# Performance work log

Hardware: AMD Instinct MI355X
Metric: run time of the kernel (lower is better)

## Reference

```python
import jax, jax.numpy as jnp
import numpy as np

K = 1024        # knowledge_num == feature dim == number of knowledge nodes
E_N = 30000     # exercise_num
E_DIR = 65536
E_UND = 65536
E_EK = 120000


def _uniform(k, shape, scale):
    return jax.random.uniform(k, shape, jnp.float32, -scale, scale)


def setup_inputs() -> dict:
    key = jax.random.key(0)
    ks = jax.random.split(key, 20)
    s = 1.0 / np.sqrt(K)        # nn.Linear default init bound
    s2 = 1.0 / np.sqrt(2 * K)
    return {
        'exer_emb': jax.random.normal(ks[0], (E_N, K), jnp.float32),
        'kn_emb': jax.random.normal(ks[1], (K, K), jnp.float32),
        'dir_src': jax.random.randint(ks[2], (E_DIR,), 0, K),
        'dir_dst': jax.random.randint(ks[3], (E_DIR,), 0, K),
        'und_src': jax.random.randint(ks[4], (E_UND,), 0, K),
        'und_dst': jax.random.randint(ks[5], (E_UND,), 0, K),
        # e_from_k: src are knowledge nodes offset into combined [exer; kn] graph
        'ek_src': jax.random.randint(ks[6], (E_EK,), 0, K) + E_N,
        'ek_dst': jax.random.randint(ks[7], (E_EK,), 0, E_N),
        'W_dir': _uniform(ks[8], (K, K), s),
        'a_dir': _uniform(ks[9], (2 * K,), s2),
        'W_und': _uniform(ks[10], (K, K), s),
        'a_und': _uniform(ks[11], (2 * K,), s2),
        'W_ek': _uniform(ks[12], (K, K), s),
        'a_ek': _uniform(ks[13], (2 * K,), s2),
        'k_w1': _uniform(ks[14], (2 * K,), s2), 'k_b1': _uniform(ks[15], (), s2),
        'k_w2': _uniform(ks[16], (2 * K,), s2), 'k_b2': _uniform(ks[17], (), s2),
        'e_w1': _uniform(ks[18], (2 * K,), s2), 'e_b1': _uniform(ks[19], (), s2),
    }


def gat_layer(h, W, a, src, dst, num_nodes):
    """GraphLayer: z = h@W; e_ij = a^T [z_src, z_dst]; softmax over in-edges; h_i = sum alpha*z_src."""
    z = h @ W                                   # [N, D]
    d = z.shape[1]
    e = (z @ a[:d])[src] + (z @ a[d:])[dst]     # [E] edge logits (split avoids [E,2D] concat)
    m = jax.ops.segment_max(e, dst, num_segments=num_nodes)
    ex = jnp.exp(e - m[dst])
    den = jax.ops.segment_sum(ex, dst, num_segments=num_nodes)
    alpha = ex / den[dst]                       # per-dst softmax (mailbox softmax)
    return jax.ops.segment_sum(alpha[:, None] * z[src], dst, num_segments=num_nodes)


def reference(exer_emb, kn_emb, dir_src, dir_dst, und_src, und_dst, ek_src, ek_dst,
              W_dir, a_dir, W_und, a_und, W_ek, a_ek,
              k_w1, k_b1, k_w2, k_b2, e_w1, e_b1):
    k_directed = gat_layer(kn_emb, W_dir, a_dir, dir_src, dir_dst, K)
    k_undirected = gat_layer(kn_emb, W_und, a_und, und_src, und_dst, K)
    e_k = jnp.concatenate([exer_emb, kn_emb], axis=0)           # [E_N+K, K]
    e_from_k = gat_layer(e_k, W_ek, a_ek, ek_src, ek_dst, E_N + K)

    # knowledge gating: softmax over two concat-linear scores
    A, B, C = kn_emb, k_directed, k_undirected
    s1 = A @ k_w1[:K] + B @ k_w1[K:] + k_b1                     # [K]
    s2 = A @ k_w2[:K] + C @ k_w2[K:] + k_b2
    sc = jax.nn.softmax(jnp.stack([s1, s2], axis=1), axis=1)    # [K, 2]
    kn_out = A + sc[:, 0:1] * B + sc[:, 1:2] * C

    # exercise gating: raw linear score (no softmax)
    Be = e_from_k[:E_N]
    se = exer_emb @ e_w1[:K] + Be @ e_w1[K:] + e_b1             # [E_N]
    exer_out = exer_emb + se[:, None] * Be
    return (exer_out, kn_out)
```

## Files before the change

### kernel.cpp

```cpp
#include <hip/hip_runtime.h>

#define E_N 30000
#define KDIM 1024
#define E_DIRN 65536
#define E_UNDN 65536
#define E_EKN 120000
#define NB (1024 + 1024 + E_N)
#define TOT_E (E_DIRN + E_UNDN + E_EKN)
#define ZERON (3 * KDIM + NB)
#define CAPK 192
#define CAPE 48
#define EKBASE (2048 * CAPK)
#define NEDGE_SLOTS (EKBASE + E_N * CAPE)

typedef __attribute__((ext_vector_type(8))) short bfrag8;
typedef __attribute__((ext_vector_type(4))) float facc4;
typedef __attribute__((ext_vector_type(4))) float f4v;

static __device__ __forceinline__ unsigned short f2bf(float f) {
    unsigned int u = __float_as_uint(f);
    u += 0x7fffu + ((u >> 16) & 1u);
    return (unsigned short)(u >> 16);
}
static __device__ __forceinline__ unsigned int pack2(float lo, float hi) {
    return (unsigned int)f2bf(lo) | ((unsigned int)f2bf(hi) << 16);
}
static __device__ __forceinline__ float bf2f(short u) {
    return __uint_as_float(((unsigned int)(unsigned short)u) << 16);
}
static __device__ __forceinline__ float dot4(f4v a, f4v b) {
    return a.x * b.x + a.y * b.y + a.z * b.z + a.w * b.w;
}
static __device__ __forceinline__ void gload16(const void* g, void* l) {
    __builtin_amdgcn_global_load_lds(
        (const __attribute__((address_space(1))) unsigned int*)g,
        (__attribute__((address_space(3))) unsigned int*)l, 16, 0, 0);
}

__global__ __launch_bounds__(256) void prep(
    const float* __restrict__ kn, const float* __restrict__ W0,
    const float* __restrict__ W1, const float* __restrict__ W2,
    unsigned short* __restrict__ knb, unsigned short* __restrict__ Wtall,
    int* __restrict__ zero_base)
{
    int z = blockIdx.z;
    int tx = threadIdx.x, ty = threadIdx.y;
    if (z == 4) {
        int idx = (blockIdx.y * 32 + blockIdx.x) * 256 + ty * 32 + tx;
        if (idx < ZERON) zero_base[idx] = 0;
        return;
    }
    if (z == 3) {
        int b = blockIdx.y * 32 + blockIdx.x;
        int t = ty * 32 + tx;
        int idx = b * 1024 + t * 4;
        float4 a = *(const float4*)&kn[idx];
        uint2 o; o.x = pack2(a.x, a.y); o.y = pack2(a.z, a.w);
        *(uint2*)&knb[idx] = o;
        return;
    }
    const float* W = (z == 0) ? W0 : (z == 1) ? W1 : W2;
    unsigned short* Wt = Wtall + (size_t)z * KDIM * KDIM;
    __shared__ float tile[32][33];
    int nb = blockIdx.x * 32, kb = blockIdx.y * 32;
#pragma unroll
    for (int r0 = 0; r0 < 32; r0 += 8)
        tile[r0 + ty][tx] = W[(size_t)(kb + r0 + ty) * KDIM + nb + tx];
    __syncthreads();
#pragma unroll
    for (int r0 = 0; r0 < 32; r0 += 8)
        Wt[(size_t)(nb + r0 + ty) * KDIM + kb + tx] = f2bf(tile[tx][r0 + ty]);
}

__global__ __launch_bounds__(256) void gemm_mfma(
    const unsigned short* __restrict__ Ab,
    const unsigned short* __restrict__ Btall,
    const float* __restrict__ a_dir, const float* __restrict__ a_und,
    const float* __restrict__ a_ek,
    unsigned short* __restrict__ Zb, float* __restrict__ zdot)
{
    int z = blockIdx.z;
    const unsigned short* Bb = Btall + (size_t)z * KDIM * KDIM;
    unsigned short* C = Zb + (size_t)z * KDIM * KDIM;
    const float* avec = (z == 0) ? a_dir : (z == 1) ? a_und : a_ek;
    __shared__ alignas(16) unsigned short As[2][64 * 64];
    __shared__ alignas(16) unsigned short Bs[2][128 * 64];
    int tid = threadIdx.x;
    int lane = tid & 63, wv = tid >> 6;
    int wr = wv >> 1, wc = wv & 1;
    int tm = blockIdx.x * 64, tn = blockIdx.y * 128;
    int srow = lane >> 3, sch = lane & 7;
    facc4 acc[2][4] = {};

    auto stage = [&](int buf, int kk) {
#pragma unroll
        for (int t = 0; t < 2; ++t) {
            int r0 = wv * 16 + t * 8;
            int row = r0 + srow;
            gload16(&Ab[(size_t)(tm + row) * KDIM + kk + ((sch ^ (row & 7)) << 3)],
                    &As[buf][r0 * 64]);
        }
#pragma unroll
        for (int t = 0; t < 4; ++t) {
            int r0 = wv * 32 + t * 8;
            int row = r0 + srow;
            gload16(&Bb[(size_t)(tn + row) * KDIM + kk + ((sch ^ (row & 7)) << 3)],
                    &Bs[buf][r0 * 64]);
        }
    };
    auto compute = [&](int buf) {
#pragma unroll
        for (int ks = 0; ks < 2; ++ks) {
            bfrag8 af[2], bfr[4];
            int kch = ks * 4 + (lane >> 4);
#pragma unroll
            for (int f = 0; f < 2; ++f) {
                int ar = wr * 32 + f * 16 + (lane & 15);
                af[f] = *(const bfrag8*)&As[buf][ar * 64 + ((kch ^ (ar & 7)) << 3)];
            }
#pragma unroll
            for (int f = 0; f < 4; ++f) {
                int bcol = wc * 64 + f * 16 + (lane & 15);
                bfr[f] = *(const bfrag8*)&Bs[buf][bcol * 64 + ((kch ^ (bcol & 7)) << 3)];
            }
#pragma unroll
            for (int i = 0; i < 2; ++i)
#pragma unroll
                for (int j = 0; j < 4; ++j)
                    acc[i][j] = __builtin_amdgcn_mfma_f32_16x16x32_bf16(af[i], bfr[j], acc[i][j], 0, 0, 0);
        }
    };

    stage(0, 0);
    __syncthreads();
    int cur = 0;
    for (int kk = 64; kk < KDIM; kk += 64) {
        stage(cur ^ 1, kk);
        compute(cur);
        __syncthreads();
        cur ^= 1;
    }
    compute(cur);

    int col0 = lane & 15, r0 = (lane >> 4) * 4;
    float av4[4];
#pragma unroll
    for (int j = 0; j < 4; ++j) av4[j] = avec[tn + wc * 64 + j * 16 + col0];
#pragma unroll
    for (int i = 0; i < 2; ++i)
#pragma unroll
        for (int j = 0; j < 4; ++j) {
            int row = tm + wr * 32 + i * 16 + r0;
            int col = tn + wc * 64 + j * 16 + col0;
#pragma unroll
            for (int r = 0; r < 4; ++r)
                C[(size_t)(row + r) * KDIM + col] = f2bf(acc[i][j][r]);
        }
#pragma unroll
    for (int i = 0; i < 2; ++i)
#pragma unroll
        for (int r = 0; r < 4; ++r) {
            float t = acc[i][0][r] * av4[0] + acc[i][1][r] * av4[1]
                    + acc[i][2][r] * av4[2] + acc[i][3][r] * av4[3];
            t += __shfl_xor(t, 1); t += __shfl_xor(t, 2);
            t += __shfl_xor(t, 4); t += __shfl_xor(t, 8);
            if ((lane & 15) == 0)
                atomicAdd(&zdot[z * KDIM + tm + wr * 32 + i * 16 + r0 + r], t);
        }
}

__global__ __launch_bounds__(256) void scatter_edges(
    const int* __restrict__ dir_src, const int* __restrict__ dir_dst,
    const int* __restrict__ und_src, const int* __restrict__ und_dst,
    const int* __restrict__ ek_src, const int* __restrict__ ek_dst,
    const float* __restrict__ zdot, int* __restrict__ counts,
    int2* __restrict__ edge_sw)
{
    int i = blockIdx.x * 256 + threadIdx.x;
    int bin, s; float w;
    if (i < E_DIRN) { bin = dir_dst[i]; s = dir_src[i]; w = expf(zdot[s]); }
    else if (i < E_DIRN + E_UNDN) {
        int loc = i - E_DIRN; bin = 1024 + und_dst[loc]; s = und_src[loc]; w = expf(zdot[1024 + s]);
    } else if (i < TOT_E) {
        int loc = i - E_DIRN - E_UNDN; bin = 2048 + ek_dst[loc]; s = ek_src[loc] - E_N; w = expf(zdot[2048 + s]);
    } else return;
    int slot = atomicAdd(&counts[bin], 1);
    if (bin < 2048) {
        if (slot < CAPK) edge_sw[(size_t)bin * CAPK + slot] = make_int2(s, __float_as_int(w));
    } else {
        if (slot < CAPE) edge_sw[EKBASE + (size_t)(bin - 2048) * CAPE + slot] = make_int2(s, __float_as_int(w));
    }
}

__global__ __launch_bounds__(256) void gather_all(
    const unsigned short* __restrict__ Zb, const int2* __restrict__ edge_sw,
    const int* __restrict__ counts,
    const float* __restrict__ exer, const float* __restrict__ kn,
    const float* __restrict__ k_w1, const float* __restrict__ k_b1,
    const float* __restrict__ k_w2, const float* __restrict__ k_b2,
    const float* __restrict__ e_w1, const float* __restrict__ e_b1,
    float* __restrict__ out)
{
    __shared__ float bcs[2][KDIM];
    __shared__ float parts[4];
    int tid = threadIdx.x;
    if (blockIdx.x < KDIM) {
        int row = blockIdx.x;
        int wv = tid >> 6, lane = tid & 63;
        int g = wv >> 1, half = wv & 1;
        int bin = (g << 10) + row;
        int n = min(counts[bin], CAPK);
        size_t start = (size_t)bin * CAPK;
        const bfrag8* Zp = (const bfrag8*)(Zb + (size_t)g * KDIM * KDIM) + half * 64 + lane;
        float b8[8] = {};
        float den = 0.f;
        for (int c0 = 0; c0 < n; c0 += 64) {
            int m = min(64, n - c0);
            int s = 0; float w = 0.f;
            if (lane < m) {
                int2 ew = edge_sw[start + c0 + lane];
                s = ew.x; w = __int_as_float(ew.y);
            }
            int j = 0;
            for (; j + 4 <= m; j += 4) {
                int   s0 = __shfl(s, j), s1 = __shfl(s, j+1), s2 = __shfl(s, j+2), s3 = __shfl(s, j+3);
                float w0 = __shfl(w, j), w1 = __shfl(w, j+1), w2 = __shfl(w, j+2), w3 = __shfl(w, j+3);
                bfrag8 v0 = Zp[(size_t)s0 * 128], v1 = Zp[(size_t)s1 * 128];
                bfrag8 v2 = Zp[(size_t)s2 * 128], v3 = Zp[(size_t)s3 * 128];
#pragma unroll
                for (int k = 0; k < 8; ++k)
                    b8[k] += w0*bf2f(v0[k]) + w1*bf2f(v1[k]) + w2*bf2f(v2[k]) + w3*bf2f(v3[k]);
                den += w0 + w1 + w2 + w3;
            }
            for (; j + 2 <= m; j += 2) {
                int   s0 = __shfl(s, j), s1 = __shfl(s, j+1);
                float w0 = __shfl(w, j), w1 = __shfl(w, j+1);
                bfrag8 v0 = Zp[(size_t)s0 * 128], v1 = Zp[(size_t)s1 * 128];
#pragma unroll
                for (int k = 0; k < 8; ++k) b8[k] += w0*bf2f(v0[k]) + w1*bf2f(v1[k]);
                den += w0 + w1;
            }
            if (j < m) {
                int   s0 = __shfl(s, j);
                float w0 = __shfl(w, j);
                bfrag8 v0 = Zp[(size_t)s0 * 128];
#pragma unroll
                for (int k = 0; k < 8; ++k) b8[k] += w0*bf2f(v0[k]);
                den += w0;
            }
        }
        float inv = (n > 0) ? 1.f / den : 0.f;
#pragma unroll
        for (int k = 0; k < 8; ++k) b8[k] *= inv;
        const float* wvp = g ? k_w2 : k_w1;
        int cb = half * 512 + lane * 8;
        f4v A0 = *(const f4v*)&kn[(size_t)row * KDIM + cb];
        f4v A1 = *(const f4v*)&kn[(size_t)row * KDIM + cb + 4];
        f4v wa0 = *(const f4v*)&wvp[cb];
        f4v wa1 = *(const f4v*)&wvp[cb + 4];
        f4v wb0 = *(const f4v*)&wvp[KDIM + cb];
        f4v wb1 = *(const f4v*)&wvp[KDIM + cb + 4];
        f4v bb0 = {b8[0], b8[1], b8[2], b8[3]};
        f4v bb1 = {b8[4], b8[5], b8[6], b8[7]};
        float p = dot4(A0, wa0) + dot4(A1, wa1) + dot4(bb0, wb0) + dot4(bb1, wb1);
#pragma unroll
        for (int off = 32; off > 0; off >>= 1) p += __shfl_xor(p, off);
        if (lane == 0) parts[wv] = p;
        *(f4v*)&bcs[g][cb] = bb0;
        *(f4v*)&bcs[g][cb + 4] = bb1;
        __syncthreads();
        float s1 = parts[0] + parts[1] + k_b1[0];
        float s2 = parts[2] + parts[3] + k_b2[0];
        float mx = fmaxf(s1, s2);
        float e1 = expf(s1 - mx), e2 = expf(s2 - mx);
        float isum = 1.f / (e1 + e2);
        float sc0 = e1 * isum, sc1 = e2 * isum;
        int col = tid * 4;
        f4v A = *(const f4v*)&kn[(size_t)row * KDIM + col];
        f4v B = *(const f4v*)&bcs[0][col];
        f4v Cc = *(const f4v*)&bcs[1][col];
        *(f4v*)&out[(size_t)(E_N + row) * KDIM + col] = A + sc0 * B + sc1 * Cc;
        return;
    }
    int row = ((blockIdx.x - KDIM) * 256 + tid) >> 6;
    int lane = tid & 63;
    int n = min(counts[2048 + row], CAPE);
    size_t start = EKBASE + (size_t)row * CAPE;
    const f4v* xr = (const f4v*)&exer[(size_t)row * KDIM];
    f4v x00 = __builtin_nontemporal_load(xr + 2 * lane);
    f4v x01 = __builtin_nontemporal_load(xr + 2 * lane + 1);
    f4v x10 = __builtin_nontemporal_load(xr + 2 * lane + 128);
    f4v x11 = __builtin_nontemporal_load(xr + 2 * lane + 129);
    const bfrag8* Zp = (const bfrag8*)(Zb + (size_t)2 * KDIM * KDIM);
    float b0[8] = {}, b1[8] = {};
    float den = 0.f;
    {
        int s = 0; float w = 0.f;
        if (lane < n) {
            int2 ew = edge_sw[start + lane];
            s = ew.x; w = __int_as_float(ew.y);
        }
        int j = 0;
        for (; j + 4 <= n; j += 4) {
            int   s0 = __shfl(s, j), s1 = __shfl(s, j+1), s2 = __shfl(s, j+2), s3 = __shfl(s, j+3);
            float w0 = __shfl(w, j), w1 = __shfl(w, j+1), w2 = __shfl(w, j+2), w3 = __shfl(w, j+3);
            const bfrag8* z0 = Zp + (size_t)s0 * 128;
            const bfrag8* z1 = Zp + (size_t)s1 * 128;
            const bfrag8* z2 = Zp + (size_t)s2 * 128;
            const bfrag8* z3 = Zp + (size_t)s3 * 128;
            bfrag8 a0 = z0[lane], a1 = z0[lane + 64];
            bfrag8 c0v = z1[lane], c1 = z1[lane + 64];
            bfrag8 d0 = z2[lane], d1 = z2[lane + 64];
            bfrag8 e0 = z3[lane], e1 = z3[lane + 64];
#pragma unroll
            for (int k = 0; k < 8; ++k) {
                b0[k] += w0*bf2f(a0[k]) + w1*bf2f(c0v[k]) + w2*bf2f(d0[k]) + w3*bf2f(e0[k]);
                b1[k] += w0*bf2f(a1[k]) + w1*bf2f(c1[k]) + w2*bf2f(d1[k]) + w3*bf2f(e1[k]);
            }
            den += w0 + w1 + w2 + w3;
        }
        for (; j + 2 <= n; j += 2) {
            int   s0 = __shfl(s, j), s1 = __shfl(s, j+1);
            float w0 = __shfl(w, j), w1 = __shfl(w, j+1);
            const bfrag8* z0 = Zp + (size_t)s0 * 128;
            const bfrag8* z1 = Zp + (size_t)s1 * 128;
            bfrag8 a0 = z0[lane], a1 = z0[lane + 64];
            bfrag8 c0v = z1[lane], c1 = z1[lane + 64];
#pragma unroll
            for (int k = 0; k < 8; ++k) {
                b0[k] += w0*bf2f(a0[k]) + w1*bf2f(c0v[k]);
                b1[k] += w0*bf2f(a1[k]) + w1*bf2f(c1[k]);
            }
            den += w0 + w1;
        }
        if (j < n) {
            int   s0 = __shfl(s, j);
            float w0 = __shfl(w, j);
            const bfrag8* z0 = Zp + (size_t)s0 * 128;
            bfrag8 a0 = z0[lane], a1 = z0[lane + 64];
#pragma unroll
            for (int k = 0; k < 8; ++k) {
                b0[k] += w0*bf2f(a0[k]);
                b1[k] += w0*bf2f(a1[k]);
            }
            den += w0;
        }
    }
    float inv = (n > 0) ? 1.f / den : 0.f;
#pragma unroll
    for (int k = 0; k < 8; ++k) { b0[k] *= inv; b1[k] *= inv; }
    const f4v* wap = (const f4v*)e_w1;
    const f4v* wbp = (const f4v*)(e_w1 + KDIM);
    f4v wa0 = wap[2*lane], wa1 = wap[2*lane+1], wa2 = wap[2*lane+128], wa3 = wap[2*lane+129];
    f4v wb0 = wbp[2*lane], wb1 = wbp[2*lane+1], wb2 = wbp[2*lane+128], wb3 = wbp[2*lane+129];
    f4v bb0 = {b0[0], b0[1], b0[2], b0[3]};
    f4v bb1 = {b0[4], b0[5], b0[6], b0[7]};
    f4v bb2 = {b1[0], b1[1], b1[2], b1[3]};
    f4v bb3 = {b1[4], b1[5], b1[6], b1[7]};
    float p = dot4(x00, wa0) + dot4(x01, wa1) + dot4(x10, wa2) + dot4(x11, wa3)
            + dot4(bb0, wb0) + dot4(bb1, wb1) + dot4(bb2, wb2) + dot4(bb3, wb3);
#pragma unroll
    for (int off = 32; off > 0; off >>= 1) p += __shfl_xor(p, off);
    float se = p + e_b1[0];
    f4v* op = (f4v*)&out[(size_t)row * KDIM];
    __builtin_nontemporal_store(x00 + se * bb0, op + 2 * lane);
    __builtin_nontemporal_store(x01 + se * bb1, op + 2 * lane + 1);
    __builtin_nontemporal_store(x10 + se * bb2, op + 2 * lane + 128);
    __builtin_nontemporal_store(x11 + se * bb3, op + 2 * lane + 129);
}

extern "C" void kernel_launch(void* const* d_in, const int* in_sizes, int n_in,
                              void* d_out, int out_size, void* d_ws, size_t ws_size,
                              hipStream_t stream)
{
    (void)in_sizes; (void)n_in; (void)out_size; (void)ws_size;
    const float* exer  = (const float*)d_in[0];
    const float* kn    = (const float*)d_in[1];
    const int* dir_src = (const int*)d_in[2];
    const int* dir_dst = (const int*)d_in[3];
    const int* und_src = (const int*)d_in[4];
    const int* und_dst = (const int*)d_in[5];
    const int* ek_src  = (const int*)d_in[6];
    const int* ek_dst  = (const int*)d_in[7];
    const float* W_dir = (const float*)d_in[8];
    const float* a_dir = (const float*)d_in[9];
    const float* W_und = (const float*)d_in[10];
    const float* a_und = (const float*)d_in[11];
    const float* W_ek  = (const float*)d_in[12];
    const float* a_ek  = (const float*)d_in[13];
    const float* k_w1  = (const float*)d_in[14];
    const float* k_b1  = (const float*)d_in[15];
    const float* k_w2  = (const float*)d_in[16];
    const float* k_b2  = (const float*)d_in[17];
    const float* e_w1  = (const float*)d_in[18];
    const float* e_b1  = (const float*)d_in[19];

    char* ws = (char*)d_ws;
    unsigned short* Zb = (unsigned short*)ws; ws += (size_t)3 * KDIM * KDIM * 2;
    float* zdot    = (float*)ws; ws += 3 * KDIM * 4;
    int* counts    = (int*)ws;   ws += NB * 4;
    int2* edge_sw  = (int2*)ws;  ws += (size_t)NEDGE_SLOTS * 8;
    unsigned short* knb = (unsigned short*)ws; ws += (size_t)KDIM * KDIM * 2;
    unsigned short* Wtb = (unsigned short*)ws; ws += (size_t)3 * KDIM * KDIM * 2;

    prep<<<dim3(32, 32, 5), dim3(32, 8), 0, stream>>>(kn, W_dir, W_und, W_ek,
                                                      knb, Wtb, (int*)zdot);
    gemm_mfma<<<dim3(16, 8, 3), 256, 0, stream>>>(knb, Wtb, a_dir, a_und, a_ek,
                                                  Zb, zdot);
    int eb = (TOT_E + 255) / 256;
    scatter_edges<<<eb, 256, 0, stream>>>(dir_src, dir_dst, und_src, und_dst,
                                          ek_src, ek_dst, zdot, counts, edge_sw);

    float* out = (float*)d_out;
    gather_all<<<KDIM + 7500, 256, 0, stream>>>(Zb, edge_sw, counts,
                                                exer, kn, k_w1, k_b1, k_w2, k_b2,
                                                e_w1, e_b1, out);
}
```

Baseline: 133.0 us.

## Process two exercise rows per wave and read edge pairs as int4 with prefetch

The gather kernel now loads edge (src, weight) pairs two at a time as int4 straight from memory, prefetching the next pair, in place of the lane-load plus shuffle broadcast scheme. This applies to both the knowledge and the exercise paths. Each wave in the exercise path now handles two rows at once, which halves the grid and gives more independent loads in flight per wave. The cost is higher register pressure and divergence when the two rows have different edge counts, plus a dependent serial chain of edge loads.

```diff
diff --git a/kernel.cpp b/kernel.cpp
--- a/kernel.cpp
+++ b/kernel.cpp
@@ -210,42 +210,26 @@
         int g = wv >> 1, half = wv & 1;
         int bin = (g << 10) + row;
         int n = min(counts[bin], CAPK);
-        size_t start = (size_t)bin * CAPK;
+        const int4* ep = (const int4*)(edge_sw + (size_t)bin * CAPK);
         const bfrag8* Zp = (const bfrag8*)(Zb + (size_t)g * KDIM * KDIM) + half * 64 + lane;
         float b8[8] = {};
         float den = 0.f;
-        for (int c0 = 0; c0 < n; c0 += 64) {
-            int m = min(64, n - c0);
-            int s = 0; float w = 0.f;
-            if (lane < m) {
-                int2 ew = edge_sw[start + c0 + lane];
-                s = ew.x; w = __int_as_float(ew.y);
-            }
-            int j = 0;
-            for (; j + 4 <= m; j += 4) {
-                int   s0 = __shfl(s, j), s1 = __shfl(s, j+1), s2 = __shfl(s, j+2), s3 = __shfl(s, j+3);
-                float w0 = __shfl(w, j), w1 = __shfl(w, j+1), w2 = __shfl(w, j+2), w3 = __shfl(w, j+3);
-                bfrag8 v0 = Zp[(size_t)s0 * 128], v1 = Zp[(size_t)s1 * 128];
-                bfrag8 v2 = Zp[(size_t)s2 * 128], v3 = Zp[(size_t)s3 * 128];
-#pragma unroll
-                for (int k = 0; k < 8; ++k)
-                    b8[k] += w0*bf2f(v0[k]) + w1*bf2f(v1[k]) + w2*bf2f(v2[k]) + w3*bf2f(v3[k]);
-                den += w0 + w1 + w2 + w3;
-            }
-            for (; j + 2 <= m; j += 2) {
-                int   s0 = __shfl(s, j), s1 = __shfl(s, j+1);
-                float w0 = __shfl(w, j), w1 = __shfl(w, j+1);
-                bfrag8 v0 = Zp[(size_t)s0 * 128], v1 = Zp[(size_t)s1 * 128];
-#pragma unroll
-                for (int k = 0; k < 8; ++k) b8[k] += w0*bf2f(v0[k]) + w1*bf2f(v1[k]);
+        int np = (n + 1) >> 1;
+        int4 cur = (np > 0) ? ep[0] : make_int4(0, 0, 0, 0);
+        for (int j = 0; j < np; ++j) {
+            int4 c = cur;
+            if (j + 1 < np) cur = ep[j + 1];
+            int s0 = c.x; float w0 = __int_as_float(c.y);
+            bfrag8 v0 = Zp[(size_t)s0 * 128];
+            if (2 * j + 1 < n) {
+                int s1 = c.z; float w1 = __int_as_float(c.w);
+                bfrag8 v1 = Zp[(size_t)s1 * 128];
+#pragma unroll
+                for (int k = 0; k < 8; ++k) b8[k] += w0 * bf2f(v0[k]) + w1 * bf2f(v1[k]);
                 den += w0 + w1;
-            }
-            if (j < m) {
-                int   s0 = __shfl(s, j);
-                float w0 = __shfl(w, j);
-                bfrag8 v0 = Zp[(size_t)s0 * 128];
-#pragma unroll
-                for (int k = 0; k < 8; ++k) b8[k] += w0*bf2f(v0[k]);
+            } else {
+#pragma unroll
+                for (int k = 0; k < 8; ++k) b8[k] += w0 * bf2f(v0[k]);
                 den += w0;
             }
         }
@@ -282,91 +266,118 @@
         *(f4v*)&out[(size_t)(E_N + row) * KDIM + col] = A + sc0 * B + sc1 * Cc;
         return;
     }
-    int row = ((blockIdx.x - KDIM) * 256 + tid) >> 6;
+    int pair = ((blockIdx.x - KDIM) * 256 + tid) >> 6;
     int lane = tid & 63;
-    int n = min(counts[2048 + row], CAPE);
-    size_t start = EKBASE + (size_t)row * CAPE;
-    const f4v* xr = (const f4v*)&exer[(size_t)row * KDIM];
-    f4v x00 = __builtin_nontemporal_load(xr + 2 * lane);
-    f4v x01 = __builtin_nontemporal_load(xr + 2 * lane + 1);
-    f4v x10 = __builtin_nontemporal_load(xr + 2 * lane + 128);
-    f4v x11 = __builtin_nontemporal_load(xr + 2 * lane + 129);
+    int rA = pair * 2, rB = rA + 1;
+    int nA = min(counts[2048 + rA], CAPE);
+    int nB = min(counts[2048 + rB], CAPE);
+    const int4* eA = (const int4*)(edge_sw + EKBASE + (size_t)rA * CAPE);
+    const int4* eB = (const int4*)(edge_sw + EKBASE + (size_t)rB * CAPE);
+    int npA = (nA + 1) >> 1, npB = (nB + 1) >> 1;
+    int npm = max(npA, npB);
+    int4 curA = (npA > 0) ? eA[0] : make_int4(0, 0, 0, 0);
+    int4 curB = (npB > 0) ? eB[0] : make_int4(0, 0, 0, 0);
+    const f4v* xrA = (const f4v*)&exer[(size_t)rA * KDIM];
+    const f4v* xrB = (const f4v*)&exer[(size_t)rB * KDIM];
+    f4v xA0 = __builtin_nontemporal_load(xrA + 2 * lane);
+    f4v xA1 = __builtin_nontemporal_load(xrA + 2 * lane + 1);
+    f4v xA2 = __builtin_nontemporal_load(xrA + 2 * lane + 128);
+    f4v xA3 = __builtin_nontemporal_load(xrA + 2 * lane + 129);
+    f4v xB0 = __builtin_nontemporal_load(xrB + 2 * lane);
+    f4v xB1 = __builtin_nontemporal_load(xrB + 2 * lane + 1);
+    f4v xB2 = __builtin_nontemporal_load(xrB + 2 * lane + 128);
+    f4v xB3 = __builtin_nontemporal_load(xrB + 2 * lane + 129);
     const bfrag8* Zp = (const bfrag8*)(Zb + (size_t)2 * KDIM * KDIM);
-    float b0[8] = {}, b1[8] = {};
-    float den = 0.f;
-    {
-        int s = 0; float w = 0.f;
-        if (lane < n) {
-            int2 ew = edge_sw[start + lane];
-            s = ew.x; w = __int_as_float(ew.y);
-        }
-        int j = 0;
-        for (; j + 4 <= n; j += 4) {
-            int   s0 = __shfl(s, j), s1 = __shfl(s, j+1), s2 = __shfl(s, j+2), s3 = __shfl(s, j+3);
-            float w0 = __shfl(w, j), w1 = __shfl(w, j+1), w2 = __shfl(w, j+2), w3 = __shfl(w, j+3);
+    float a0[8] = {}, a1[8] = {}, b0[8] = {}, b1[8] = {};
+    float denA = 0.f, denB = 0.f;
+    for (int j = 0; j < npm; ++j) {
+        int4 cA = curA, cB = curB;
+        if (j + 1 < npA) curA = eA[j + 1];
+        if (j + 1 < npB) curB = eB[j + 1];
+        if (j < npA) {
+            int s0 = cA.x; float w0 = __int_as_float(cA.y);
             const bfrag8* z0 = Zp + (size_t)s0 * 128;
-            const bfrag8* z1 = Zp + (size_t)s1 * 128;
-            const bfrag8* z2 = Zp + (size_t)s2 * 128;
-            const bfrag8* z3 = Zp + (size_t)s3 * 128;
-            bfrag8 a0 = z0[lane], a1 = z0[lane + 64];
-            bfrag8 c0v = z1[lane], c1 = z1[lane + 64];
-            bfrag8 d0 = z2[lane], d1 = z2[lane + 64];
-            bfrag8 e0 = z3[lane], e1 = z3[lane + 64];
-#pragma unroll
-            for (int k = 0; k < 8; ++k) {
-                b0[k] += w0*bf2f(a0[k]) + w1*bf2f(c0v[k]) + w2*bf2f(d0[k]) + w3*bf2f(e0[k]);
-                b1[k] += w0*bf2f(a1[k]) + w1*bf2f(c1[k]) + w2*bf2f(d1[k]) + w3*bf2f(e1[k]);
+            bfrag8 v00 = z0[lane], v01 = z0[lane + 64];
+            if (2 * j + 1 < nA) {
+                int s1 = cA.z; float w1 = __int_as_float(cA.w);
+                const bfrag8* z1 = Zp + (size_t)s1 * 128;
+                bfrag8 v10 = z1[lane], v11 = z1[lane + 64];
+#pragma unroll
+                for (int k = 0; k < 8; ++k) {
+                    a0[k] += w0 * bf2f(v00[k]) + w1 * bf2f(v10[k]);
+                    a1[k] += w0 * bf2f(v01[k]) + w1 * bf2f(v11[k]);
+                }
+                denA += w0 + w1;
+            } else {
+#pragma unroll
+                for (int k = 0; k < 8; ++k) {
+                    a0[k] += w0 * bf2f(v00[k]);
+                    a1[k] += w0 * bf2f(v01[k]);
+                }
+                denA += w0;
             }
-            den += w0 + w1 + w2 + w3;
-        }
-        for (; j + 2 <= n; j += 2) {
-            int   s0 = __shfl(s, j), s1 = __shfl(s, j+1);
-            float w0 = __shfl(w, j), w1 = __shfl(w, j+1);
+        }
+        if (j < npB) {
+            int s0 = cB.x; float w0 = __int_as_float(cB.y);
             const bfrag8* z0 = Zp + (size_t)s0 * 128;
-            const bfrag8* z1 = Zp + (size_t)s1 * 128;
-            bfrag8 a0 = z0[lane], a1 = z0[lane + 64];
-            bfrag8 c0v = z1[lane], c1 = z1[lane + 64];
-#pragma unroll
-            for (int k = 0; k < 8; ++k) {
-                b0[k] += w0*bf2f(a0[k]) + w1*bf2f(c0v[k]);
-                b1[k] += w0*bf2f(a1[k]) + w1*bf2f(c1[k]);
+            bfrag8 v00 = z0[lane], v01 = z0[lane + 64];
+            if (2 * j + 1 < nB) {
+                int s1 = cB.z; float w1 = __int_as_float(cB.w);
+                const bfrag8* z1 = Zp + (size_t)s1 * 128;
+                bfrag8 v10 = z1[lane], v11 = z1[lane + 64];
+#pragma unroll
+                for (int k = 0; k < 8; ++k) {
+                    b0[k] += w0 * bf2f(v00[k]) + w1 * bf2f(v10[k]);
+                    b1[k] += w0 * bf2f(v01[k]) + w1 * bf2f(v11[k]);
+                }
+                denB += w0 + w1;
+            } else {
+#pragma unroll
+                for (int k = 0; k < 8; ++k) {
+                    b0[k] += w0 * bf2f(v00[k]);
+                    b1[k] += w0 * bf2f(v01[k]);
+                }
+                denB += w0;
             }
-            den += w0 + w1;
-        }
-        if (j < n) {
-            int   s0 = __shfl(s, j);
-            float w0 = __shfl(w, j);
-            const bfrag8* z0 = Zp + (size_t)s0 * 128;
-            bfrag8 a0 = z0[lane], a1 = z0[lane + 64];
-#pragma unroll
-            for (int k = 0; k < 8; ++k) {
-                b0[k] += w0*bf2f(a0[k]);
-                b1[k] += w0*bf2f(a1[k]);
-            }
-            den += w0;
-        }
-    }
-    float inv = (n > 0) ? 1.f / den : 0.f;
-#pragma unroll
-    for (int k = 0; k < 8; ++k) { b0[k] *= inv; b1[k] *= inv; }
+        }
+    }
+    float invA = (nA > 0) ? 1.f / denA : 0.f;
+    float invB = (nB > 0) ? 1.f / denB : 0.f;
+#pragma unroll
+    for (int k = 0; k < 8; ++k) { a0[k] *= invA; a1[k] *= invA; b0[k] *= invB; b1[k] *= invB; }
     const f4v* wap = (const f4v*)e_w1;
     const f4v* wbp = (const f4v*)(e_w1 + KDIM);
     f4v wa0 = wap[2*lane], wa1 = wap[2*lane+1], wa2 = wap[2*lane+128], wa3 = wap[2*lane+129];
     f4v wb0 = wbp[2*lane], wb1 = wbp[2*lane+1], wb2 = wbp[2*lane+128], wb3 = wbp[2*lane+129];
-    f4v bb0 = {b0[0], b0[1], b0[2], b0[3]};
-    f4v bb1 = {b0[4], b0[5], b0[6], b0[7]};
-    f4v bb2 = {b1[0], b1[1], b1[2], b1[3]};
-    f4v bb3 = {b1[4], b1[5], b1[6], b1[7]};
-    float p = dot4(x00, wa0) + dot4(x01, wa1) + dot4(x10, wa2) + dot4(x11, wa3)
-            + dot4(bb0, wb0) + dot4(bb1, wb1) + dot4(bb2, wb2) + dot4(bb3, wb3);
-#pragma unroll
-    for (int off = 32; off > 0; off >>= 1) p += __shfl_xor(p, off);
-    float se = p + e_b1[0];
-    f4v* op = (f4v*)&out[(size_t)row * KDIM];
-    __builtin_nontemporal_store(x00 + se * bb0, op + 2 * lane);
-    __builtin_nontemporal_store(x01 + se * bb1, op + 2 * lane + 1);
-    __builtin_nontemporal_store(x10 + se * bb2, op + 2 * lane + 128);
-    __builtin_nontemporal_store(x11 + se * bb3, op + 2 * lane + 129);
+    f4v aa0 = {a0[0], a0[1], a0[2], a0[3]};
+    f4v aa1 = {a0[4], a0[5], a0[6], a0[7]};
+    f4v aa2 = {a1[0], a1[1], a1[2], a1[3]};
+    f4v aa3 = {a1[4], a1[5], a1[6], a1[7]};
+    f4v ba0 = {b0[0], b0[1], b0[2], b0[3]};
+    f4v ba1 = {b0[4], b0[5], b0[6], b0[7]};
+    f4v ba2 = {b1[0], b1[1], b1[2], b1[3]};
+    f4v ba3 = {b1[4], b1[5], b1[6], b1[7]};
+    float pA = dot4(xA0, wa0) + dot4(xA1, wa1) + dot4(xA2, wa2) + dot4(xA3, wa3)
+             + dot4(aa0, wb0) + dot4(aa1, wb1) + dot4(aa2, wb2) + dot4(aa3, wb3);
+    float pB = dot4(xB0, wa0) + dot4(xB1, wa1) + dot4(xB2, wa2) + dot4(xB3, wa3)
+             + dot4(ba0, wb0) + dot4(ba1, wb1) + dot4(ba2, wb2) + dot4(ba3, wb3);
+#pragma unroll
+    for (int off = 32; off > 0; off >>= 1) {
+        pA += __shfl_xor(pA, off);
+        pB += __shfl_xor(pB, off);
+    }
+    float seA = pA + e_b1[0];
+    float seB = pB + e_b1[0];
+    f4v* opA = (f4v*)&out[(size_t)rA * KDIM];
+    f4v* opB = (f4v*)&out[(size_t)rB * KDIM];
+    __builtin_nontemporal_store(xA0 + seA * aa0, opA + 2 * lane);
+    __builtin_nontemporal_store(xA1 + seA * aa1, opA + 2 * lane + 1);
+    __builtin_nontemporal_store(xA2 + seA * aa2, opA + 2 * lane + 128);
+    __builtin_nontemporal_store(xA3 + seA * aa3, opA + 2 * lane + 129);
+    __builtin_nontemporal_store(xB0 + seB * ba0, opB + 2 * lane);
+    __builtin_nontemporal_store(xB1 + seB * ba1, opB + 2 * lane + 1);
+    __builtin_nontemporal_store(xB2 + seB * ba2, opB + 2 * lane + 128);
+    __builtin_nontemporal_store(xB3 + seB * ba3, opB + 2 * lane + 129);
 }
 
 extern "C" void kernel_launch(void* const* d_in, const int* in_sizes, int n_in,
@@ -412,7 +423,7 @@
                                           ek_src, ek_dst, zdot, counts, edge_sw);
 
     float* out = (float*)d_out;
-    gather_all<<<KDIM + 7500, 256, 0, stream>>>(Zb, edge_sw, counts,
+    gather_all<<<KDIM + 3750, 256, 0, stream>>>(Zb, edge_sw, counts,
                                                 exer, kn, k_w1, k_b1, k_w2, k_b2,
                                                 e_w1, e_b1, out);
 }
```

Result: slower. 156.6 us (+17.8%).
